# Optimization experiments

Hardware: AMD Instinct MI355X
Metric: run time of the kernel (lower is better)

Reference implementation:

```python
import jax, jax.numpy as jnp
import numpy as np

N_NODES = 50000      # also number of hyperedges (square incidence)
N_HEDGES = 50000
N_INC = 800000       # number of (node, hyperedge) incidences
N_LINKS = 20000
IN_DIM = 128         # edge_x dim; x dim is 2*IN_DIM
LATENT = [64, 64, 64]
HIDDEN = 256


def _hconv(x, src, dst, n_src, n_dst, W, b):
    """PyG HypergraphConv (no attention, unit hyperedge weights):
    out = D^{-1} H B^{-1} H^T (x W) + b, with src=node idx, dst=hyperedge idx."""
    xw = x @ W  # [n_src, out]
    ones = jnp.ones(src.shape[0], xw.dtype)
    Bdeg = jax.ops.segment_sum(ones, dst, num_segments=n_dst)
    Binv = jnp.where(Bdeg > 0, 1.0 / Bdeg, 0.0)
    Ddeg = jax.ops.segment_sum(ones, src, num_segments=n_src)
    Dinv = jnp.where(Ddeg > 0, 1.0 / Ddeg, 0.0)
    # node -> hyperedge aggregate, normalized by B^{-1}
    he = jax.ops.segment_sum(xw[src], dst, num_segments=n_dst) * Binv[:, None]
    # hyperedge -> node aggregate, normalized by D^{-1}
    out = jax.ops.segment_sum(he[dst], src, num_segments=n_src) * Dinv[:, None]
    return out + b


def setup_inputs() -> dict:
    key = jax.random.key(0)
    ks = jax.random.split(key, 24)
    inp = {
        "x": jax.random.normal(ks[0], (N_NODES, 2 * IN_DIM), jnp.float32),
        "edge_x": jax.random.normal(ks[1], (N_HEDGES, IN_DIM), jnp.float32),
        "edge_index": jax.random.randint(ks[2], (2, N_INC), 0, N_NODES, dtype=jnp.int32),
        "marks": jax.random.randint(ks[3], (N_LINKS,), 0, N_NODES, dtype=jnp.int32),
        "edge_marks": jax.random.randint(ks[4], (N_LINKS,), 0, N_HEDGES - 1, dtype=jnp.int32),
    }
    def lin(k, fin, fout):
        s = 1.0 / np.sqrt(fin)
        return jax.random.uniform(k, (fin, fout), jnp.float32, -s, s)
    # node convs: (2*IN_DIM -> 2*L0), (2*L0 -> 2*L1), (2*L1 -> 2*L2)
    nd = [2 * IN_DIM] + [2 * l for l in LATENT]
    ed = [IN_DIM] + list(LATENT)
    for i in range(3):
        inp[f"Wn{i}"] = lin(ks[5 + i], nd[i], nd[i + 1])
        inp[f"bn{i}"] = jnp.zeros((nd[i + 1],), jnp.float32)
        inp[f"We{i}"] = lin(ks[8 + i], ed[i], ed[i + 1])
        inp[f"be{i}"] = jnp.zeros((ed[i + 1],), jnp.float32)
    feat = sum(LATENT) * 4
    inp["W1"] = lin(ks[11], feat, HIDDEN)
    inp["b1"] = jnp.zeros((HIDDEN,), jnp.float32)
    inp["W2"] = lin(ks[12], HIDDEN, 2)
    inp["b2"] = jnp.zeros((2,), jnp.float32)
    return inp


def reference(x, edge_x, edge_index, marks, edge_marks,
              Wn0, bn0, Wn1, bn1, Wn2, bn2,
              We0, be0, We1, be1, We2, be2,
              W1, b1, W2, b2):
    nsrc, hdst = edge_index[0], edge_index[1]
    node_layers = [(Wn0, bn0), (Wn1, bn1), (Wn2, bn2)]
    edge_layers = [(We0, be0), (We1, be1), (We2, be2)]
    h, all_x = x, []
    for W, b in node_layers:
        h = jax.nn.relu(_hconv(h, nsrc, hdst, N_NODES, N_HEDGES, W, b))
        all_x.append(h)
    g, all_e = edge_x, []
    for W, b in edge_layers:  # flipped incidence: hyperedges act as nodes
        g = jax.nn.relu(_hconv(g, hdst, nsrc, N_HEDGES, N_NODES, W, b))
        all_e.append(g)
    xc = jnp.concatenate(all_x, axis=1)[marks]           # [L, 2*sum(latent)]
    ec = jnp.concatenate(all_e, axis=1)                  # [M, sum(latent)]
    a, b2_ = ec[edge_marks], ec[edge_marks + 1]
    feat = jnp.concatenate([jnp.minimum(a, b2_), jnp.maximum(a, b2_), xc], axis=1)
    h1 = jax.nn.relu(feat @ W1 + b1)
    logits = h1 @ W2 + b2
    return jax.nn.log_softmax(logits, axis=1)
```

## Files before the change

kernel.cpp:

```cpp
#include <hip/hip_runtime.h>
#include <hip/hip_fp16.h>
#include <math.h>

#define NN 50000
#define NH 50000
#define NI 800000
#define NL 20000

using half8 = __attribute__((ext_vector_type(8))) _Float16;
using f32x4 = __attribute__((ext_vector_type(4))) float;

static __device__ __forceinline__ float2 pack_h4(float4 v) {
    float2 st;
    *(__half2*)&st.x = __float22half2_rn(make_float2(v.x, v.y));
    *(__half2*)&st.y = __float22half2_rn(make_float2(v.z, v.w));
    return st;
}
static __device__ __forceinline__ void acc_h8(float4& a, float4& b, float4 raw) {
    const __half2* hp = (const __half2*)&raw;
    float2 f0 = __half22float2(hp[0]);
    float2 f1 = __half22float2(hp[1]);
    float2 f2 = __half22float2(hp[2]);
    float2 f3 = __half22float2(hp[3]);
    a.x += f0.x; a.y += f0.y; a.z += f1.x; a.w += f1.y;
    b.x += f2.x; b.y += f2.y; b.z += f3.x; b.w += f3.y;
}
static __device__ __forceinline__ float4 pack_h8(float4 a, float4 b) {
    float4 st;
    ((__half2*)&st)[0] = __float22half2_rn(make_float2(a.x, a.y));
    ((__half2*)&st)[1] = __float22half2_rn(make_float2(a.z, a.w));
    ((__half2*)&st)[2] = __float22half2_rn(make_float2(b.x, b.y));
    ((__half2*)&st)[3] = __float22half2_rn(make_float2(b.z, b.w));
    return st;
}

#define WT_BLKS 1088
#define HIST_SEGS 98
#define HIST_PER  8164
__global__ void k_prep(const float* __restrict__ Wn0, const float* __restrict__ Wn1,
                       const float* __restrict__ Wn2, const float* __restrict__ We0,
                       const float* __restrict__ We1, const float* __restrict__ We2,
                       const float* __restrict__ W1,
                       __half* __restrict__ Wnt0, __half* __restrict__ Wnt1,
                       __half* __restrict__ Wnt2, __half* __restrict__ Wet0,
                       __half* __restrict__ Wet1, __half* __restrict__ Wet2,
                       __half* __restrict__ W1t,
                       const int* __restrict__ ei, int* __restrict__ cnt_n,
                       int* __restrict__ cnt_h) {
    int b = blockIdx.x, t = threadIdx.x;
    if (b < WT_BLKS) {
        int u = b * 256 + t;
        if (u < 278528) {
            const float* S; __half* D; int K, N;
            if (u < 32768)      { S = Wn0; D = Wnt0; K = 256; N = 128; }
            else if (u < 49152) { S = Wn1; D = Wnt1; K = 128; N = 128; u -= 32768; }
            else if (u < 65536) { S = Wn2; D = Wnt2; K = 128; N = 128; u -= 49152; }
            else if (u < 73728) { S = We0; D = Wet0; K = 128; N = 64;  u -= 65536; }
            else if (u < 77824) { S = We1; D = Wet1; K = 64;  N = 64;  u -= 73728; }
            else if (u < 81920) { S = We2; D = Wet2; K = 64;  N = 64;  u -= 77824; }
            else                { S = W1;  D = W1t;  K = 768; N = 256; u -= 81920; }
            int n = u / K, k = u % K;
            D[(size_t)n * K + k] = __float2half(S[(size_t)k * N + n]);
        }
    } else {
        int hb = b - WT_BLKS;
        int bucket = hb & 7;
        int seg = hb >> 3;
        int lo = seg * HIST_PER;
        int hi = min(lo + HIST_PER, NI);
        for (int e = lo + t; e < hi; e += 256) {
            int s = ei[e], d = ei[e + NI];
            if (s / 6250 == bucket) atomicAdd(&cnt_n[s], 1);
            if (d / 6250 == bucket) atomicAdd(&cnt_h[d], 1);
        }
    }
}

__global__ void k_scanp1(const int* __restrict__ cnt_n, const int* __restrict__ cnt_h,
                         int* __restrict__ parts) {
    __shared__ int s[256];
    int arr = blockIdx.x / 196, blk = blockIdx.x % 196, t = threadIdx.x;
    const int* cnt = arr ? cnt_h : cnt_n;
    int i = blk * 256 + t;
    int v = (i < 50000) ? cnt[i] : 0;
    s[t] = v;
    __syncthreads();
#pragma unroll
    for (int d = 128; d > 0; d >>= 1) {
        if (t < d) s[t] += s[t + d];
        __syncthreads();
    }
    if (t == 0) parts[arr * 256 + blk] = s[0];
}

__global__ void k_scanp2(int* __restrict__ parts, int* __restrict__ off_n,
                         int* __restrict__ off_h) {
    __shared__ int s[256];
    int b = blockIdx.x, t = threadIdx.x;
    int* P = parts + b * 256;
    int v = (t < 196) ? P[t] : 0;
    s[t] = v;
    __syncthreads();
#pragma unroll
    for (int d = 1; d < 256; d <<= 1) {
        int u = (t >= d) ? s[t - d] : 0;
        __syncthreads();
        s[t] += u;
        __syncthreads();
    }
    if (t < 196) P[t] = s[t] - v;
    if (t == 0) {
        int* off = b ? off_h : off_n;
        off[50000] = s[255];
    }
}

__global__ void k_scanp3(const int* __restrict__ cnt_n, const int* __restrict__ cnt_h,
                         const int* __restrict__ parts, int* __restrict__ off_n,
                         int* __restrict__ off_h, float* __restrict__ invn,
                         float* __restrict__ invh) {
    __shared__ int s[256];
    int arr = blockIdx.x / 196, blk = blockIdx.x % 196, t = threadIdx.x;
    const int* cnt = arr ? cnt_h : cnt_n;
    int* off = arr ? off_h : off_n;
    float* inv = arr ? invh : invn;
    int i = blk * 256 + t;
    int c = (i < 50000) ? cnt[i] : 0;
    s[t] = c;
    __syncthreads();
#pragma unroll
    for (int d = 1; d < 256; d <<= 1) {
        int u = (t >= d) ? s[t - d] : 0;
        __syncthreads();
        s[t] += u;
        __syncthreads();
    }
    if (i < 50000) {
        off[i] = parts[arr * 256 + blk] + s[t] - c;
        inv[i] = c > 0 ? 1.0f / (float)c : 0.0f;
    }
}

#define FILL_SEGS 98
#define FILL_PER  8164
__global__ void k_fill(const int* __restrict__ ei, const int* __restrict__ off_n,
                       const int* __restrict__ off_h, int* __restrict__ cur_n,
                       int* __restrict__ cur_h, int* __restrict__ adj_n,
                       int* __restrict__ adj_h) {
    int bucket = blockIdx.x & 7;
    int seg = blockIdx.x >> 3;
    int lo = seg * FILL_PER;
    int hi = min(lo + FILL_PER, NI);
    for (int e = lo + (int)threadIdx.x; e < hi; e += 256) {
        int s = ei[e], d = ei[e + NI];
        if (d / 6250 == bucket) {
            int p = atomicAdd(&cur_h[d], 1);
            adj_h[off_h[d] + p] = s;
        }
        if (s / 6250 == bucket) {
            int q = atomicAdd(&cur_n[s], 1);
            adj_n[off_n[s] + q] = d;
        }
    }
}

template <typename SrcT, int BM, int BN, int FM, int FN>
static __device__ __forceinline__ void gemm_body(const SrcT* __restrict__ X,
                                                 const __half* __restrict__ Wt,
                                                 __half* __restrict__ Y, int M, int K,
                                                 int blk, __half* smem) {
    constexpr int LDK = 56;
    constexpr int WN = BN / 4;
    __half* Xs = smem;
    __half* Ws = smem + BM * LDK;
    int t = threadIdx.x;
    int wave = t >> 6, lane = t & 63;
    int g = lane >> 4, lr = lane & 15;
    int bm0 = blk * BM;
    f32x4 acc[FM][FN] = {};

    for (int k0 = 0; k0 < K; k0 += 32) {
        for (int u = t; u < BM * 4; u += 256) {
            int r = u >> 2, q = u & 3;
            int rg = bm0 + r; if (rg >= M) rg = M - 1;
            if constexpr (sizeof(SrcT) == 4) {
                const float* src = (const float*)X + (size_t)rg * K + k0 + q * 8;
                float4 v0 = *(const float4*)src;
                float4 v1 = *(const float4*)(src + 4);
                *(float2*)&Xs[r * LDK + q * 8]     = pack_h4(v0);
                *(float2*)&Xs[r * LDK + q * 8 + 4] = pack_h4(v1);
            } else {
                *(float4*)&Xs[r * LDK + q * 8] =
                    *(const float4*)((const __half*)X + (size_t)rg * K + k0 + q * 8);
            }
        }
        for (int u = t; u < BN * 4; u += 256) {
            int r = u >> 2, q = u & 3;
            *(float4*)&Ws[r * LDK + q * 8] = *(const float4*)&Wt[(size_t)r * K + k0 + q * 8];
        }
        __syncthreads();
        half8 a[FM], b[FN];
#pragma unroll
        for (int fm = 0; fm < FM; fm++)
            a[fm] = *(const half8*)&Xs[(fm * 16 + lr) * LDK + g * 8];
#pragma unroll
        for (int fn = 0; fn < FN; fn++)
            b[fn] = *(const half8*)&Ws[(wave * WN + fn * 16 + lr) * LDK + g * 8];
#pragma unroll
        for (int fm = 0; fm < FM; fm++)
#pragma unroll
            for (int fn = 0; fn < FN; fn++)
                acc[fm][fn] = __builtin_amdgcn_mfma_f32_16x16x32_f16(a[fm], b[fn], acc[fm][fn], 0, 0, 0);
        __syncthreads();
    }
#pragma unroll
    for (int fm = 0; fm < FM; fm++) {
#pragma unroll
        for (int fn = 0; fn < FN; fn++) {
            int cg = wave * WN + fn * 16 + lr;
#pragma unroll
            for (int reg = 0; reg < 4; reg++) {
                int rg = bm0 + fm * 16 + g * 4 + reg;
                if (rg < M) Y[(size_t)rg * BN + cg] = __float2half(acc[fm][fn][reg]);
            }
        }
    }
}

template <typename SrcT>
__global__ void __launch_bounds__(256)
k_gemm2(const SrcT* __restrict__ Xn, const __half* __restrict__ Wtn,
        __half* __restrict__ Yn, int Kn,
        const SrcT* __restrict__ Xe, const __half* __restrict__ Wte,
        __half* __restrict__ Ye, int Ke) {
    __shared__ __align__(16) __half smem[(64 + 128) * 56];
    if (blockIdx.x < 782)
        gemm_body<SrcT, 64, 128, 4, 2>(Xn, Wtn, Yn, NN, Kn, blockIdx.x, smem);
    else
        gemm_body<SrcT, 64, 64, 4, 1>(Xe, Wte, Ye, NH, Ke, blockIdx.x - 782, smem);
}

template <int F, bool RELU>
static __device__ __forceinline__ void pull_body(const __half* __restrict__ in,
                                                 const int* __restrict__ off,
                                                 const int* __restrict__ adj,
                                                 const float* __restrict__ scale,
                                                 const float* __restrict__ bias,
                                                 __half* __restrict__ out,
                                                 int nrows, int blk) {
    constexpr int TPR = F / 8;
    constexpr int RPB = 256 / TPR;
    int r = blk * RPB + (int)threadIdx.x / TPR;
    int lane = threadIdx.x % TPR;
    if (r >= nrows) return;
    int lo = off[r], hi = off[r + 1];
    const float4* in4 = (const float4*)in;
    float4 a0 = {0,0,0,0}, b0 = {0,0,0,0}, a1 = {0,0,0,0}, b1v = {0,0,0,0};
    float4 a2 = {0,0,0,0}, b2v = {0,0,0,0}, a3 = {0,0,0,0}, b3 = {0,0,0,0};
    int j = lo;
    for (; j + 7 < hi; j += 8) {
        int c0 = adj[j], c1 = adj[j + 1], c2 = adj[j + 2], c3 = adj[j + 3];
        int c4 = adj[j + 4], c5 = adj[j + 5], c6 = adj[j + 6], c7 = adj[j + 7];
        float4 v0 = in4[(size_t)c0 * TPR + lane];
        float4 v1 = in4[(size_t)c1 * TPR + lane];
        float4 v2 = in4[(size_t)c2 * TPR + lane];
        float4 v3 = in4[(size_t)c3 * TPR + lane];
        float4 v4 = in4[(size_t)c4 * TPR + lane];
        float4 v5 = in4[(size_t)c5 * TPR + lane];
        float4 v6 = in4[(size_t)c6 * TPR + lane];
        float4 v7 = in4[(size_t)c7 * TPR + lane];
        acc_h8(a0, b0, v0); acc_h8(a1, b1v, v1); acc_h8(a2, b2v, v2); acc_h8(a3, b3, v3);
        acc_h8(a0, b0, v4); acc_h8(a1, b1v, v5); acc_h8(a2, b2v, v6); acc_h8(a3, b3, v7);
    }
    for (; j + 1 < hi; j += 2) {
        int c0 = adj[j], c1 = adj[j + 1];
        float4 v0 = in4[(size_t)c0 * TPR + lane];
        float4 v1 = in4[(size_t)c1 * TPR + lane];
        acc_h8(a0, b0, v0); acc_h8(a1, b1v, v1);
    }
    if (j < hi) {
        float4 v0 = in4[(size_t)adj[j] * TPR + lane];
        acc_h8(a0, b0, v0);
    }
    a0.x += a1.x + a2.x + a3.x; a0.y += a1.y + a2.y + a3.y;
    a0.z += a1.z + a2.z + a3.z; a0.w += a1.w + a2.w + a3.w;
    b0.x += b1v.x + b2v.x + b3.x; b0.y += b1v.y + b2v.y + b3.y;
    b0.z += b1v.z + b2v.z + b3.z; b0.w += b1v.w + b2v.w + b3.w;
    float sc = scale[r];
    if (RELU) {
        float4 ba = ((const float4*)bias)[lane * 2];
        float4 bb = ((const float4*)bias)[lane * 2 + 1];
        a0.x = fmaxf(fmaf(a0.x, sc, ba.x), 0.f);
        a0.y = fmaxf(fmaf(a0.y, sc, ba.y), 0.f);
        a0.z = fmaxf(fmaf(a0.z, sc, ba.z), 0.f);
        a0.w = fmaxf(fmaf(a0.w, sc, ba.w), 0.f);
        b0.x = fmaxf(fmaf(b0.x, sc, bb.x), 0.f);
        b0.y = fmaxf(fmaf(b0.y, sc, bb.y), 0.f);
        b0.z = fmaxf(fmaf(b0.z, sc, bb.z), 0.f);
        b0.w = fmaxf(fmaf(b0.w, sc, bb.w), 0.f);
    } else {
        a0.x *= sc; a0.y *= sc; a0.z *= sc; a0.w *= sc;
        b0.x *= sc; b0.y *= sc; b0.z *= sc; b0.w *= sc;
    }
    ((float4*)out)[(size_t)r * TPR + lane] = pack_h8(a0, b0);
}

template <bool RELU>
__global__ void k_pull2(const __half* __restrict__ inA, const int* __restrict__ offA,
                        const int* __restrict__ adjA, const float* __restrict__ scA,
                        const float* __restrict__ biA, __half* __restrict__ outA, int rowsA,
                        const __half* __restrict__ inB, const int* __restrict__ offB,
                        const int* __restrict__ adjB, const float* __restrict__ scB,
                        const float* __restrict__ biB, __half* __restrict__ outB, int rowsB) {
    if (blockIdx.x < 3125)
        pull_body<128, RELU>(inA, offA, adjA, scA, biA, outA, rowsA, blockIdx.x);
    else
        pull_body<64, RELU>(inB, offB, adjB, scB, biB, outB, rowsB, blockIdx.x - 3125);
}

__global__ void __launch_bounds__(256)
k_mlp_mfma(const __half* __restrict__ hx1, const __half* __restrict__ hx2,
           const __half* __restrict__ hx3, const __half* __restrict__ gx1,
           const __half* __restrict__ gx2, const __half* __restrict__ gx3,
           const int* __restrict__ marks, const int* __restrict__ emarks,
           const __half* __restrict__ W1t, const float* __restrict__ b1,
           const float* __restrict__ W2, const float* __restrict__ b2,
           float* __restrict__ out) {
    constexpr int LDK = 56;
    __shared__ __align__(16) __half Xs[32 * LDK];
    __shared__ __align__(16) __half Ws[256 * LDK];
    __shared__ float part[4][32][2];
    int t = threadIdx.x;
    int wave = t >> 6, lane = t & 63;
    int g = lane >> 4, lr = lane & 15;
    int bm0 = blockIdx.x * 32;
    int r_s = t >> 2, q_s = t & 3;
    int m_s = 0, e_s = 0;
    if (t < 128) {
        int l = bm0 + r_s; if (l >= NL) l = NL - 1;
        m_s = marks[l]; e_s = emarks[l];
    }
    f32x4 acc[2][4] = {};

    for (int k0 = 0; k0 < 768; k0 += 32) {
        if (t < 128) {
            if (k0 < 384) {
                int fb = (k0 < 192 ? k0 : k0 - 192) + q_s * 8;
                const __half* gs = fb < 64 ? gx1 : (fb < 128 ? gx2 : gx3);
                int off = fb & 63;
                half8 va = *(const half8*)&gs[(size_t)e_s * 64 + off];
                half8 vb = *(const half8*)&gs[(size_t)(e_s + 1) * 64 + off];
                half8 rv;
                if (k0 < 192) {
#pragma unroll
                    for (int j = 0; j < 8; j++)
                        rv[j] = (_Float16)fminf((float)va[j], (float)vb[j]);
                } else {
#pragma unroll
                    for (int j = 0; j < 8; j++)
                        rv[j] = (_Float16)fmaxf((float)va[j], (float)vb[j]);
                }
                *(half8*)&Xs[r_s * LDK + q_s * 8] = rv;
            } else {
                int fb = (k0 - 384) + q_s * 8;
                const __half* hs = fb < 128 ? hx1 : (fb < 256 ? hx2 : hx3);
                int off = fb & 127;
                *(float4*)&Xs[r_s * LDK + q_s * 8] = *(const float4*)&hs[(size_t)m_s * 128 + off];
            }
        }
        for (int u = t; u < 1024; u += 256) {
            int r = u >> 2, q = u & 3;
            *(float4*)&Ws[r * LDK + q * 8] = *(const float4*)&W1t[(size_t)r * 768 + k0 + q * 8];
        }
        __syncthreads();
        half8 a[2], b[4];
#pragma unroll
        for (int fm = 0; fm < 2; fm++)
            a[fm] = *(const half8*)&Xs[(fm * 16 + lr) * LDK + g * 8];
#pragma unroll
        for (int fn = 0; fn < 4; fn++)
            b[fn] = *(const half8*)&Ws[(wave * 64 + fn * 16 + lr) * LDK + g * 8];
#pragma unroll
        for (int fm = 0; fm < 2; fm++)
#pragma unroll
            for (int fn = 0; fn < 4; fn++)
                acc[fm][fn] = __builtin_amdgcn_mfma_f32_16x16x32_f16(a[fm], b[fn], acc[fm][fn], 0, 0, 0);
        __syncthreads();
    }
    float b1c[4], w20[4], w21[4];
#pragma unroll
    for (int fn = 0; fn < 4; fn++) {
        int col = wave * 64 + fn * 16 + lr;
        b1c[fn] = b1[col];
        w20[fn] = W2[(size_t)col * 2 + 0];
        w21[fn] = W2[(size_t)col * 2 + 1];
    }
    float p0[2][4], p1[2][4];
#pragma unroll
    for (int fm = 0; fm < 2; fm++) {
#pragma unroll
        for (int reg = 0; reg < 4; reg++) {
            float s0 = 0.f, s1 = 0.f;
#pragma unroll
            for (int fn = 0; fn < 4; fn++) {
                float hh = fmaxf(acc[fm][fn][reg] + b1c[fn], 0.f);
                s0 = fmaf(hh, w20[fn], s0);
                s1 = fmaf(hh, w21[fn], s1);
            }
            p0[fm][reg] = s0; p1[fm][reg] = s1;
        }
    }
#pragma unroll
    for (int mask = 1; mask < 16; mask <<= 1) {
#pragma unroll
        for (int fm = 0; fm < 2; fm++)
#pragma unroll
            for (int reg = 0; reg < 4; reg++) {
                p0[fm][reg] += __shfl_xor(p0[fm][reg], mask);
                p1[fm][reg] += __shfl_xor(p1[fm][reg], mask);
            }
    }
    if (lr == 0) {
#pragma unroll
        for (int fm = 0; fm < 2; fm++)
#pragma unroll
            for (int reg = 0; reg < 4; reg++) {
                int row = fm * 16 + g * 4 + reg;
                part[wave][row][0] = p0[fm][reg];
                part[wave][row][1] = p1[fm][reg];
            }
    }
    __syncthreads();
    if (t < 32) {
        int l = bm0 + t;
        if (l < NL) {
            float l0 = part[0][t][0] + part[1][t][0] + part[2][t][0] + part[3][t][0] + b2[0];
            float l1 = part[0][t][1] + part[1][t][1] + part[2][t][1] + part[3][t][1] + b2[1];
            float mx = fmaxf(l0, l1);
            float lse = mx + logf(expf(l0 - mx) + expf(l1 - mx));
            out[(size_t)l * 2 + 0] = l0 - lse;
            out[(size_t)l * 2 + 1] = l1 - lse;
        }
    }
}

extern "C" void kernel_launch(void* const* d_in, const int* in_sizes, int n_in,
                              void* d_out, int out_size, void* d_ws, size_t ws_size,
                              hipStream_t stream) {
    const float* x      = (const float*)d_in[0];
    const float* ex     = (const float*)d_in[1];
    const int*   ei     = (const int*)d_in[2];
    const int*   marks  = (const int*)d_in[3];
    const int*   emarks = (const int*)d_in[4];
    const float* Wn[3] = {(const float*)d_in[5],  (const float*)d_in[9],  (const float*)d_in[13]};
    const float* bn[3] = {(const float*)d_in[6],  (const float*)d_in[10], (const float*)d_in[14]};
    const float* We[3] = {(const float*)d_in[7],  (const float*)d_in[11], (const float*)d_in[15]};
    const float* be[3] = {(const float*)d_in[8],  (const float*)d_in[12], (const float*)d_in[16]};
    const float* W1 = (const float*)d_in[17];
    const float* b1 = (const float*)d_in[18];
    const float* W2 = (const float*)d_in[19];
    const float* b2 = (const float*)d_in[20];

    int*    off_n = (int*)d_ws;
    int*    off_h = off_n + 50004;
    int*    adj_n = off_h + 50004;
    int*    adj_h = adj_n + 800000;
    int*    cnt   = adj_h + 800000;
    int*    cur   = cnt + 100000;
    int*    parts = cur + 100000;
    float*  invn  = (float*)(parts + 512);
    float*  invh  = invn + 50000;
    __half* xwb   = (__half*)(invh + 50000);
    __half* xwb2  = xwb + 6400000;
    __half* heb   = xwb2 + 3200000;
    __half* heb2  = heb + 6400000;
    __half* h[3]  = {heb2 + 3200000, heb2 + 9600000, heb2 + 16000000};
    __half* g[3]  = {h[2] + 6400000, h[2] + 9600000, h[2] + 12800000};
    __half* Wnt[3] = {g[2] + 3200000, g[2] + 3232768, g[2] + 3249152};
    __half* Wet[3] = {g[2] + 3265536, g[2] + 3273728, g[2] + 3277824};
    __half* W1t    = g[2] + 3281920;

    int* cnt_n = cnt;
    int* cnt_h = cnt + 50000;
    int* cur_n = cur;
    int* cur_h = cur + 50000;

    hipMemsetAsync(cnt, 0, 200000 * sizeof(int), stream);
    k_prep<<<WT_BLKS + HIST_SEGS * 8, 256, 0, stream>>>(
        Wn[0], Wn[1], Wn[2], We[0], We[1], We[2], W1,
        Wnt[0], Wnt[1], Wnt[2], Wet[0], Wet[1], Wet[2], W1t,
        ei, cnt_n, cnt_h);
    k_scanp1<<<392, 256, 0, stream>>>(cnt_n, cnt_h, parts);
    k_scanp2<<<2, 256, 0, stream>>>(parts, off_n, off_h);
    k_scanp3<<<392, 256, 0, stream>>>(cnt_n, cnt_h, parts, off_n, off_h, invn, invh);
    k_fill<<<FILL_SEGS * 8, 256, 0, stream>>>(ei, off_n, off_h, cur_n, cur_h, adj_n, adj_h);

    k_gemm2<float><<<1564, 256, 0, stream>>>(x, Wnt[0], xwb, 256, ex, Wet[0], xwb2, 128);
    k_pull2<false><<<4688, 256, 0, stream>>>(xwb, off_h, adj_h, invh, nullptr, heb, NH,
                                             xwb2, off_n, adj_n, invn, nullptr, heb2, NN);
    k_pull2<true><<<4688, 256, 0, stream>>>(heb, off_n, adj_n, invn, bn[0], h[0], NN,
                                            heb2, off_h, adj_h, invh, be[0], g[0], NH);
    for (int i = 1; i < 3; i++) {
        k_gemm2<__half><<<1564, 256, 0, stream>>>(h[i - 1], Wnt[i], xwb, 128,
                                                  g[i - 1], Wet[i], xwb2, 64);
        k_pull2<false><<<4688, 256, 0, stream>>>(xwb, off_h, adj_h, invh, nullptr, heb, NH,
                                                 xwb2, off_n, adj_n, invn, nullptr, heb2, NN);
        k_pull2<true><<<4688, 256, 0, stream>>>(heb, off_n, adj_n, invn, bn[i], h[i], NN,
                                                heb2, off_h, adj_h, invh, be[i], g[i], NH);
    }

    k_mlp_mfma<<<(NL + 31) / 32, 256, 0, stream>>>(h[0], h[1], h[2], g[0], g[1], g[2],
                                                   marks, emarks, W1t, b1, W2, b2, (float*)d_out);
}
```

Baseline: 571.3 us.

## Store hidden features in column-sliced layout so gathers stay cache-resident per slice

Features are stored slice-major instead of row-major: 16-half column slices for the node path and 8-half slices for the hyperedge path. The GEMM epilogue, the pull kernels and the MLP loads are all rewritten to use this layout. Each pull block now handles only one slice (blockIdx & 7), so the random gather for that slice touches a smaller array that can stay in cache. The cost is more blocks re-reading the adjacency lists and offsets, once per slice, and scattered 2-byte stores in the GEMM epilogue.

```diff
diff --git a/kernel.cpp b/kernel.cpp
--- a/kernel.cpp
+++ b/kernel.cpp
@@ -6,6 +6,7 @@
 #define NH 50000
 #define NI 800000
 #define NL 20000
+
 
 using half8 = __attribute__((ext_vector_type(8))) _Float16;
 using f32x4 = __attribute__((ext_vector_type(4))) float;
@@ -164,7 +165,7 @@
     }
 }
 
-template <typename SrcT, int BM, int BN, int FM, int FN>
+template <typename SrcT, int BM, int BN, int FM, int FN, int SCI>
 static __device__ __forceinline__ void gemm_body(const SrcT* __restrict__ X,
                                                  const __half* __restrict__ Wt,
                                                  __half* __restrict__ Y, int M, int K,
@@ -189,9 +190,15 @@
                 float4 v1 = *(const float4*)(src + 4);
                 *(float2*)&Xs[r * LDK + q * 8]     = pack_h4(v0);
                 *(float2*)&Xs[r * LDK + q * 8 + 4] = pack_h4(v1);
+            } else if constexpr (SCI == 16) {
+                int kk0 = k0 + q * 8;
+                const __half* src = (const __half*)X +
+                    (size_t)(kk0 >> 4) * ((size_t)M * 16) + (size_t)rg * 16 + (kk0 & 15);
+                *(float4*)&Xs[r * LDK + q * 8] = *(const float4*)src;
             } else {
-                *(float4*)&Xs[r * LDK + q * 8] =
-                    *(const float4*)((const __half*)X + (size_t)rg * K + k0 + q * 8);
+                const __half* src = (const __half*)X +
+                    (size_t)((k0 >> 3) + q) * ((size_t)M * 8) + (size_t)rg * 8;
+                *(float4*)&Xs[r * LDK + q * 8] = *(const float4*)src;
             }
         }
         for (int u = t; u < BN * 4; u += 256) {
@@ -217,11 +224,24 @@
     for (int fm = 0; fm < FM; fm++) {
 #pragma unroll
         for (int fn = 0; fn < FN; fn++) {
-            int cg = wave * WN + fn * 16 + lr;
-#pragma unroll
-            for (int reg = 0; reg < 4; reg++) {
-                int rg = bm0 + fm * 16 + g * 4 + reg;
-                if (rg < M) Y[(size_t)rg * BN + cg] = __float2half(acc[fm][fn][reg]);
+            __half* dst;
+            int col;
+            if constexpr (BN == 128) {
+                dst = Y + (size_t)(wave * 2 + fn) * ((size_t)M * 16);
+                col = lr;
+#pragma unroll
+                for (int reg = 0; reg < 4; reg++) {
+                    int rg = bm0 + fm * 16 + g * 4 + reg;
+                    if (rg < M) dst[(size_t)rg * 16 + col] = __float2half(acc[fm][fn][reg]);
+                }
+            } else {
+                dst = Y + (size_t)(wave * 2 + (lr >> 3)) * ((size_t)M * 8);
+                col = lr & 7;
+#pragma unroll
+                for (int reg = 0; reg < 4; reg++) {
+                    int rg = bm0 + fm * 16 + g * 4 + reg;
+                    if (rg < M) dst[(size_t)rg * 8 + col] = __float2half(acc[fm][fn][reg]);
+                }
             }
         }
     }
@@ -235,88 +255,120 @@
         __half* __restrict__ Ye, int Ke) {
     __shared__ __align__(16) __half smem[(64 + 128) * 56];
     if (blockIdx.x < 782)
-        gemm_body<SrcT, 64, 128, 4, 2>(Xn, Wtn, Yn, NN, Kn, blockIdx.x, smem);
+        gemm_body<SrcT, 64, 128, 4, 2, 16>(Xn, Wtn, Yn, NN, Kn, blockIdx.x, smem);
     else
-        gemm_body<SrcT, 64, 64, 4, 1>(Xe, Wte, Ye, NH, Ke, blockIdx.x - 782, smem);
-}
-
-template <int F, bool RELU>
-static __device__ __forceinline__ void pull_body(const __half* __restrict__ in,
-                                                 const int* __restrict__ off,
-                                                 const int* __restrict__ adj,
-                                                 const float* __restrict__ scale,
-                                                 const float* __restrict__ bias,
-                                                 __half* __restrict__ out,
-                                                 int nrows, int blk) {
-    constexpr int TPR = F / 8;
-    constexpr int RPB = 256 / TPR;
-    int r = blk * RPB + (int)threadIdx.x / TPR;
-    int lane = threadIdx.x % TPR;
-    if (r >= nrows) return;
-    int lo = off[r], hi = off[r + 1];
-    const float4* in4 = (const float4*)in;
+        gemm_body<SrcT, 64, 64, 4, 1, 8>(Xe, Wte, Ye, NH, Ke, blockIdx.x - 782, smem);
+}
+
+#define PULL_RB_A 391
+#define PULL_RB_B 196
+template <bool RELU>
+__global__ void __launch_bounds__(256)
+k_pull2(const __half* __restrict__ inA, const int* __restrict__ offA,
+        const int* __restrict__ adjA, const float* __restrict__ scA,
+        const float* __restrict__ biA, __half* __restrict__ outA,
+        const __half* __restrict__ inB, const int* __restrict__ offB,
+        const int* __restrict__ adjB, const float* __restrict__ scB,
+        const float* __restrict__ biB, __half* __restrict__ outB) {
+    int s = blockIdx.x & 7;
+    int rb = blockIdx.x >> 3;
+    int t = threadIdx.x;
     float4 a0 = {0,0,0,0}, b0 = {0,0,0,0}, a1 = {0,0,0,0}, b1v = {0,0,0,0};
     float4 a2 = {0,0,0,0}, b2v = {0,0,0,0}, a3 = {0,0,0,0}, b3 = {0,0,0,0};
-    int j = lo;
-    for (; j + 7 < hi; j += 8) {
-        int c0 = adj[j], c1 = adj[j + 1], c2 = adj[j + 2], c3 = adj[j + 3];
-        int c4 = adj[j + 4], c5 = adj[j + 5], c6 = adj[j + 6], c7 = adj[j + 7];
-        float4 v0 = in4[(size_t)c0 * TPR + lane];
-        float4 v1 = in4[(size_t)c1 * TPR + lane];
-        float4 v2 = in4[(size_t)c2 * TPR + lane];
-        float4 v3 = in4[(size_t)c3 * TPR + lane];
-        float4 v4 = in4[(size_t)c4 * TPR + lane];
-        float4 v5 = in4[(size_t)c5 * TPR + lane];
-        float4 v6 = in4[(size_t)c6 * TPR + lane];
-        float4 v7 = in4[(size_t)c7 * TPR + lane];
-        acc_h8(a0, b0, v0); acc_h8(a1, b1v, v1); acc_h8(a2, b2v, v2); acc_h8(a3, b3, v3);
-        acc_h8(a0, b0, v4); acc_h8(a1, b1v, v5); acc_h8(a2, b2v, v6); acc_h8(a3, b3, v7);
-    }
-    for (; j + 1 < hi; j += 2) {
-        int c0 = adj[j], c1 = adj[j + 1];
-        float4 v0 = in4[(size_t)c0 * TPR + lane];
-        float4 v1 = in4[(size_t)c1 * TPR + lane];
-        acc_h8(a0, b0, v0); acc_h8(a1, b1v, v1);
-    }
-    if (j < hi) {
-        float4 v0 = in4[(size_t)adj[j] * TPR + lane];
-        acc_h8(a0, b0, v0);
-    }
-    a0.x += a1.x + a2.x + a3.x; a0.y += a1.y + a2.y + a3.y;
-    a0.z += a1.z + a2.z + a3.z; a0.w += a1.w + a2.w + a3.w;
-    b0.x += b1v.x + b2v.x + b3.x; b0.y += b1v.y + b2v.y + b3.y;
-    b0.z += b1v.z + b2v.z + b3.z; b0.w += b1v.w + b2v.w + b3.w;
-    float sc = scale[r];
-    if (RELU) {
-        float4 ba = ((const float4*)bias)[lane * 2];
-        float4 bb = ((const float4*)bias)[lane * 2 + 1];
-        a0.x = fmaxf(fmaf(a0.x, sc, ba.x), 0.f);
-        a0.y = fmaxf(fmaf(a0.y, sc, ba.y), 0.f);
-        a0.z = fmaxf(fmaf(a0.z, sc, ba.z), 0.f);
-        a0.w = fmaxf(fmaf(a0.w, sc, ba.w), 0.f);
-        b0.x = fmaxf(fmaf(b0.x, sc, bb.x), 0.f);
-        b0.y = fmaxf(fmaf(b0.y, sc, bb.y), 0.f);
-        b0.z = fmaxf(fmaf(b0.z, sc, bb.z), 0.f);
-        b0.w = fmaxf(fmaf(b0.w, sc, bb.w), 0.f);
+    if (rb < PULL_RB_A) {
+        int r = rb * 128 + (t >> 1);
+        int L = t & 1;
+        if (r >= 50000) return;
+        const float4* src4 = (const float4*)inA + (size_t)s * 100000 + L;
+        int lo = offA[r], hi = offA[r + 1];
+        int j = lo;
+        for (; j + 7 < hi; j += 8) {
+            int c0 = adjA[j], c1 = adjA[j+1], c2 = adjA[j+2], c3 = adjA[j+3];
+            int c4 = adjA[j+4], c5 = adjA[j+5], c6 = adjA[j+6], c7 = adjA[j+7];
+            float4 v0 = src4[(size_t)c0 * 2];
+            float4 v1 = src4[(size_t)c1 * 2];
+            float4 v2 = src4[(size_t)c2 * 2];
+            float4 v3 = src4[(size_t)c3 * 2];
+            float4 v4 = src4[(size_t)c4 * 2];
+            float4 v5 = src4[(size_t)c5 * 2];
+            float4 v6 = src4[(size_t)c6 * 2];
+            float4 v7 = src4[(size_t)c7 * 2];
+            acc_h8(a0, b0, v0); acc_h8(a1, b1v, v1); acc_h8(a2, b2v, v2); acc_h8(a3, b3, v3);
+            acc_h8(a0, b0, v4); acc_h8(a1, b1v, v5); acc_h8(a2, b2v, v6); acc_h8(a3, b3, v7);
+        }
+        for (; j < hi; j++) {
+            float4 v0 = src4[(size_t)adjA[j] * 2];
+            acc_h8(a0, b0, v0);
+        }
+        a0.x += a1.x + a2.x + a3.x; a0.y += a1.y + a2.y + a3.y;
+        a0.z += a1.z + a2.z + a3.z; a0.w += a1.w + a2.w + a3.w;
+        b0.x += b1v.x + b2v.x + b3.x; b0.y += b1v.y + b2v.y + b3.y;
+        b0.z += b1v.z + b2v.z + b3.z; b0.w += b1v.w + b2v.w + b3.w;
+        float sc = scA[r];
+        if (RELU) {
+            float4 ba = *(const float4*)&biA[s * 16 + L * 8];
+            float4 bb = *(const float4*)&biA[s * 16 + L * 8 + 4];
+            a0.x = fmaxf(fmaf(a0.x, sc, ba.x), 0.f);
+            a0.y = fmaxf(fmaf(a0.y, sc, ba.y), 0.f);
+            a0.z = fmaxf(fmaf(a0.z, sc, ba.z), 0.f);
+            a0.w = fmaxf(fmaf(a0.w, sc, ba.w), 0.f);
+            b0.x = fmaxf(fmaf(b0.x, sc, bb.x), 0.f);
+            b0.y = fmaxf(fmaf(b0.y, sc, bb.y), 0.f);
+            b0.z = fmaxf(fmaf(b0.z, sc, bb.z), 0.f);
+            b0.w = fmaxf(fmaf(b0.w, sc, bb.w), 0.f);
+        } else {
+            a0.x *= sc; a0.y *= sc; a0.z *= sc; a0.w *= sc;
+            b0.x *= sc; b0.y *= sc; b0.z *= sc; b0.w *= sc;
+        }
+        ((float4*)outA)[(size_t)s * 100000 + (size_t)r * 2 + L] = pack_h8(a0, b0);
     } else {
-        a0.x *= sc; a0.y *= sc; a0.z *= sc; a0.w *= sc;
-        b0.x *= sc; b0.y *= sc; b0.z *= sc; b0.w *= sc;
-    }
-    ((float4*)out)[(size_t)r * TPR + lane] = pack_h8(a0, b0);
-}
-
-template <bool RELU>
-__global__ void k_pull2(const __half* __restrict__ inA, const int* __restrict__ offA,
-                        const int* __restrict__ adjA, const float* __restrict__ scA,
-                        const float* __restrict__ biA, __half* __restrict__ outA, int rowsA,
-                        const __half* __restrict__ inB, const int* __restrict__ offB,
-                        const int* __restrict__ adjB, const float* __restrict__ scB,
-                        const float* __restrict__ biB, __half* __restrict__ outB, int rowsB) {
-    if (blockIdx.x < 3125)
-        pull_body<128, RELU>(inA, offA, adjA, scA, biA, outA, rowsA, blockIdx.x);
-    else
-        pull_body<64, RELU>(inB, offB, adjB, scB, biB, outB, rowsB, blockIdx.x - 3125);
-}
+        int r = (rb - PULL_RB_A) * 256 + t;
+        if (r >= 50000) return;
+        const float4* src4 = (const float4*)inB + (size_t)s * 50000;
+        int lo = offB[r], hi = offB[r + 1];
+        int j = lo;
+        for (; j + 7 < hi; j += 8) {
+            int c0 = adjB[j], c1 = adjB[j+1], c2 = adjB[j+2], c3 = adjB[j+3];
+            int c4 = adjB[j+4], c5 = adjB[j+5], c6 = adjB[j+6], c7 = adjB[j+7];
+            float4 v0 = src4[c0];
+            float4 v1 = src4[c1];
+            float4 v2 = src4[c2];
+            float4 v3 = src4[c3];
+            float4 v4 = src4[c4];
+            float4 v5 = src4[c5];
+            float4 v6 = src4[c6];
+            float4 v7 = src4[c7];
+            acc_h8(a0, b0, v0); acc_h8(a1, b1v, v1); acc_h8(a2, b2v, v2); acc_h8(a3, b3, v3);
+            acc_h8(a0, b0, v4); acc_h8(a1, b1v, v5); acc_h8(a2, b2v, v6); acc_h8(a3, b3, v7);
+        }
+        for (; j < hi; j++) {
+            float4 v0 = src4[adjB[j]];
+            acc_h8(a0, b0, v0);
+        }
+        a0.x += a1.x + a2.x + a3.x; a0.y += a1.y + a2.y + a3.y;
+        a0.z += a1.z + a2.z + a3.z; a0.w += a1.w + a2.w + a3.w;
+        b0.x += b1v.x + b2v.x + b3.x; b0.y += b1v.y + b2v.y + b3.y;
+        b0.z += b1v.z + b2v.z + b3.z; b0.w += b1v.w + b2v.w + b3.w;
+        float sc = scB[r];
+        if (RELU) {
+            float4 ba = *(const float4*)&biB[s * 8];
+            float4 bb = *(const float4*)&biB[s * 8 + 4];
+            a0.x = fmaxf(fmaf(a0.x, sc, ba.x), 0.f);
+            a0.y = fmaxf(fmaf(a0.y, sc, ba.y), 0.f);
+            a0.z = fmaxf(fmaf(a0.z, sc, ba.z), 0.f);
+            a0.w = fmaxf(fmaf(a0.w, sc, ba.w), 0.f);
+            b0.x = fmaxf(fmaf(b0.x, sc, bb.x), 0.f);
+            b0.y = fmaxf(fmaf(b0.y, sc, bb.y), 0.f);
+            b0.z = fmaxf(fmaf(b0.z, sc, bb.z), 0.f);
+            b0.w = fmaxf(fmaf(b0.w, sc, bb.w), 0.f);
+        } else {
+            a0.x *= sc; a0.y *= sc; a0.z *= sc; a0.w *= sc;
+            b0.x *= sc; b0.y *= sc; b0.z *= sc; b0.w *= sc;
+        }
+        ((float4*)outB)[(size_t)s * 50000 + r] = pack_h8(a0, b0);
+    }
+}
+#define PULL_GRID (8 * (PULL_RB_A + PULL_RB_B))
 
 __global__ void __launch_bounds__(256)
 k_mlp_mfma(const __half* __restrict__ hx1, const __half* __restrict__ hx2,
@@ -348,8 +400,9 @@
                 int fb = (k0 < 192 ? k0 : k0 - 192) + q_s * 8;
                 const __half* gs = fb < 64 ? gx1 : (fb < 128 ? gx2 : gx3);
                 int off = fb & 63;
-                half8 va = *(const half8*)&gs[(size_t)e_s * 64 + off];
-                half8 vb = *(const half8*)&gs[(size_t)(e_s + 1) * 64 + off];
+                const __half* base = gs + (size_t)(off >> 3) * 400000;
+                half8 va = *(const half8*)&base[(size_t)e_s * 8];
+                half8 vb = *(const half8*)&base[(size_t)(e_s + 1) * 8];
                 half8 rv;
                 if (k0 < 192) {
 #pragma unroll
@@ -365,7 +418,9 @@
                 int fb = (k0 - 384) + q_s * 8;
                 const __half* hs = fb < 128 ? hx1 : (fb < 256 ? hx2 : hx3);
                 int off = fb & 127;
-                *(float4*)&Xs[r_s * LDK + q_s * 8] = *(const float4*)&hs[(size_t)m_s * 128 + off];
+                const __half* base = hs + (size_t)(off >> 4) * 800000;
+                *(float4*)&Xs[r_s * LDK + q_s * 8] =
+                    *(const float4*)&base[(size_t)m_s * 16 + (off & 15)];
             }
         }
         for (int u = t; u < 1024; u += 256) {
@@ -496,17 +551,17 @@
     k_fill<<<FILL_SEGS * 8, 256, 0, stream>>>(ei, off_n, off_h, cur_n, cur_h, adj_n, adj_h);
 
     k_gemm2<float><<<1564, 256, 0, stream>>>(x, Wnt[0], xwb, 256, ex, Wet[0], xwb2, 128);
-    k_pull2<false><<<4688, 256, 0, stream>>>(xwb, off_h, adj_h, invh, nullptr, heb, NH,
-                                             xwb2, off_n, adj_n, invn, nullptr, heb2, NN);
-    k_pull2<true><<<4688, 256, 0, stream>>>(heb, off_n, adj_n, invn, bn[0], h[0], NN,
-                                            heb2, off_h, adj_h, invh, be[0], g[0], NH);
+    k_pull2<false><<<PULL_GRID, 256, 0, stream>>>(xwb, off_h, adj_h, invh, nullptr, heb,
+                                                  xwb2, off_n, adj_n, invn, nullptr, heb2);
+    k_pull2<true><<<PULL_GRID, 256, 0, stream>>>(heb, off_n, adj_n, invn, bn[0], h[0],
+                                                 heb2, off_h, adj_h, invh, be[0], g[0]);
     for (int i = 1; i < 3; i++) {
         k_gemm2<__half><<<1564, 256, 0, stream>>>(h[i - 1], Wnt[i], xwb, 128,
                                                   g[i - 1], Wet[i], xwb2, 64);
-        k_pull2<false><<<4688, 256, 0, stream>>>(xwb, off_h, adj_h, invh, nullptr, heb, NH,
-                                                 xwb2, off_n, adj_n, invn, nullptr, heb2, NN);
-        k_pull2<true><<<4688, 256, 0, stream>>>(heb, off_n, adj_n, invn, bn[i], h[i], NN,
-                                                heb2, off_h, adj_h, invh, be[i], g[i], NH);
+        k_pull2<false><<<PULL_GRID, 256, 0, stream>>>(xwb, off_h, adj_h, invh, nullptr, heb,
+                                                      xwb2, off_n, adj_n, invn, nullptr, heb2);
+        k_pull2<true><<<PULL_GRID, 256, 0, stream>>>(heb, off_n, adj_n, invn, bn[i], h[i],
+                                                     heb2, off_h, adj_h, invh, be[i], g[i]);
     }
 
     k_mlp_mfma<<<(NL + 31) / 32, 256, 0, stream>>>(h[0], h[1], h[2], g[0], g[1], g[2],
```

Measured after the change: 680.9 us. +19.2%, slower.
